# Optimization experiments

Hardware: AMD Instinct MI355X
Metric: run time of the kernel (lower is better)

## Reference

```python
import jax, jax.numpy as jnp
import numpy as np

N = 100000          # nodes
E = 1600000         # edges
F = 128             # raw node features
D = 16              # embedding_dim (per-head out channels)
H = 8               # heads
NEG_SLOPE = 0.2     # GATConv leaky_relu slope
EPS = 1e-16         # PyG softmax denominator eps


def _glorot(key, shape):
    fan_in, fan_out = shape[0], shape[-1]
    lim = np.sqrt(6.0 / (fan_in + fan_out))
    return jax.random.uniform(key, shape, jnp.float32, -lim, lim)


def setup_inputs() -> dict:
    key = jax.random.key(0)
    ks = jax.random.split(key, 24)
    x = jax.random.normal(ks[0], (N, F), jnp.float32)
    edge_index = jax.random.randint(ks[1], (2, E), 0, N, jnp.int64)
    HD = H * D
    return {
        "x": x,
        "edge_index": edge_index,
        # attribute embedding Linear(F, D)
        "W_emb": _glorot(ks[2], (F, D)), "b_emb": jnp.zeros((D,), jnp.float32),
        # GAT layer 0: in=D, out=D per head
        "W0": _glorot(ks[3], (D, HD)),
        "as0": _glorot(ks[4], (H, D)), "ad0": _glorot(ks[5], (H, D)),
        "b0": jnp.zeros((HD,), jnp.float32),
        # GAT layer 1: in=H*D, out=D per head
        "W1": _glorot(ks[6], (HD, HD)),
        "as1": _glorot(ks[7], (H, D)), "ad1": _glorot(ks[8], (H, D)),
        "b1": jnp.zeros((HD,), jnp.float32),
        "Wy1": _glorot(ks[9], (HD, 1)), "by1": jnp.zeros((1,), jnp.float32),
        "Wy0": _glorot(ks[10], (HD, 1)), "by0": jnp.zeros((1,), jnp.float32),
        # classifier Linear(HD, D) -> ReLU -> Linear(D, 1) -> Sigmoid
        "Wc1": _glorot(ks[11], (HD, D)), "bc1": jnp.zeros((D,), jnp.float32),
        "Wc2": _glorot(ks[12], (D, 1)), "bc2": jnp.zeros((1,), jnp.float32),
    }


def _gat_conv(h, src, dst, W, att_src, att_dst, bias):
    # h: [N, in] -> out: [N, H*D]; src/dst already include self-loops
    g = (h @ W).reshape(N, H, D)                                   # [N,H,D]
    a_src = jnp.einsum('nhd,hd->nh', g, att_src)                   # [N,H]
    a_dst = jnp.einsum('nhd,hd->nh', g, att_dst)                   # [N,H]
    logits = jax.nn.leaky_relu(a_src[src] + a_dst[dst], NEG_SLOPE) # [Et,H]
    m = jax.ops.segment_max(logits, dst, num_segments=N)           # [N,H]
    ex = jnp.exp(logits - m[dst])
    denom = jax.ops.segment_sum(ex, dst, num_segments=N)           # [N,H]
    alpha = ex / (denom[dst] + EPS)                                # [Et,H]
    msg = g[src] * alpha[..., None]                                # [Et,H,D]
    out = jax.ops.segment_sum(msg, dst, num_segments=N)            # [N,H,D]
    return out.reshape(N, H * D) + bias


def reference(x, edge_index, W_emb, b_emb, W0, as0, ad0, b0,
              W1, as1, ad1, b1, Wy1, by1, Wy0, by0, Wc1, bc1, Wc2, bc2):
    # add self loops (PyG GATConv default)
    loop = jnp.arange(N, dtype=edge_index.dtype)
    src = jnp.concatenate([edge_index[0], loop])
    dst = jnp.concatenate([edge_index[1], loop])

    h = x @ W_emb + b_emb                        # [N,D]
    h = _gat_conv(h, src, dst, W0, as0, ad0, b0) # [N,H*D]
    h = _gat_conv(h, src, dst, W1, as1, ad1, b1) # [N,H*D]

    y1 = h @ Wy1 + by1
    y0 = h @ Wy0 + by0
    causal_effect = y1 - y0                      # [N,1]
    propensity = jax.nn.sigmoid(jax.nn.relu(h @ Wc1 + bc1) @ Wc2 + bc2)  # [N,1]
    return causal_effect, propensity
```

## Files before the change

kernel.cpp:

```cpp
#include <hip/hip_runtime.h>
#include <hip/hip_fp16.h>
#include <math.h>

#define N_NODES 100000
#define E_EDGES 1600000
#define F_IN 128
#define D_DIM 16
#define H_HEADS 8
#define HD 128
#define NEG_SLOPE 0.2f

#define SCAN_BLOCKS 256
#define SCAN_T 256
#define SCAN_CH ((N_NODES + SCAN_BLOCKS - 1) / SCAN_BLOCKS)

#define NTILES ((N_NODES + 63) / 64)

#define NB_E 196
#define EB 128
#define CH_E ((E_EDGES + EB - 1) / EB)

__global__ __launch_bounds__(256) void embed_kernel(
        const float* __restrict__ x, const float* __restrict__ W,
        const float* __restrict__ b, __half* __restrict__ h0) {
    __shared__ float Ws[F_IN * D_DIM];
    __shared__ float bs[D_DIM];
    __shared__ float xs[16][F_IN + 1];
    int t = threadIdx.x;
    for (int i = t; i < F_IN * D_DIM; i += 256) Ws[i] = W[i];
    if (t < D_DIM) bs[t] = b[t];
    __syncthreads();
    for (int base = blockIdx.x * 16; base < N_NODES; base += gridDim.x * 16) {
        int cnt = min(16, N_NODES - base);
        __syncthreads();
        for (int i = t; i < cnt * F_IN; i += 256) {
            int nn = i >> 7, k = i & 127;
            xs[nn][k] = x[(size_t)(base + nn) * F_IN + k];
        }
        __syncthreads();
        int nn = t >> 4, c = t & 15;
        if (nn < cnt) {
            float a0 = 0.f, a1 = 0.f, a2 = 0.f, a3 = 0.f;
            #pragma unroll
            for (int k = 0; k < F_IN; k += 4) {
                a0 += xs[nn][k + 0] * Ws[(k + 0) * D_DIM + c];
                a1 += xs[nn][k + 1] * Ws[(k + 1) * D_DIM + c];
                a2 += xs[nn][k + 2] * Ws[(k + 2) * D_DIM + c];
                a3 += xs[nn][k + 3] * Ws[(k + 3) * D_DIM + c];
            }
            h0[(size_t)(base + nn) * D_DIM + c] =
                __float2half((a0 + a1) + (a2 + a3) + bs[c]);
        }
    }
}

__global__ __launch_bounds__(256) void precompute_kernel(
        const float* __restrict__ W0, const float* __restrict__ W1,
        const float* __restrict__ as0, const float* __restrict__ ad0,
        const float* __restrict__ b0,
        float* __restrict__ W_fused, float* __restrict__ u_s,
        float* __restrict__ u_d, float* __restrict__ bvec) {
    int t = threadIdx.x;
    if (t < 128) {
        int h = t >> 4, c = t & 15;
        float ss = 0.f, sd = 0.f;
        for (int dp = 0; dp < 16; ++dp) {
            float w = W0[c * HD + h * 16 + dp];
            ss += w * as0[h * 16 + dp];
            sd += w * ad0[h * 16 + dp];
        }
        u_s[t] = ss; u_d[t] = sd;
        float bb = 0.f;
        for (int k = 0; k < HD; ++k) bb += b0[k] * W1[k * HD + t];
        bvec[t] = bb;
    }
    for (int idx = t; idx < HD * HD; idx += 256) {
        int i = idx >> 7, j = idx & 127;
        int h = i >> 4, c = i & 15;
        float s = 0.f;
        for (int dp = 0; dp < 16; ++dp)
            s += W0[c * HD + h * 16 + dp] * W1[(h * 16 + dp) * HD + j];
        W_fused[idx] = s;
    }
}

__global__ __launch_bounds__(256) void attdot0_kernel(
        const __half* __restrict__ h0, const float* __restrict__ u_s,
        const float* __restrict__ u_d,
        float* __restrict__ a_s, float* __restrict__ a_d) {
    __shared__ float us[128], ud[128];
    int t = threadIdx.x;
    if (t < 128) { us[t] = u_s[t]; ud[t] = u_d[t]; }
    __syncthreads();
    int gidx = blockIdx.x * 256 + t;
    int n = gidx >> 3, h = gidx & 7;
    if (n >= N_NODES) return;
    const __half2* hp = (const __half2*)(h0 + (size_t)n * D_DIM);
    float ss = 0.f, sd = 0.f;
    #pragma unroll
    for (int c2 = 0; c2 < 8; ++c2) {
        float2 f = __half22float2(hp[c2]);
        ss += f.x * us[h * 16 + 2 * c2] + f.y * us[h * 16 + 2 * c2 + 1];
        sd += f.x * ud[h * 16 + 2 * c2] + f.y * ud[h * 16 + 2 * c2 + 1];
    }
    a_s[n * 8 + h] = ss;
    a_d[n * 8 + h] = sd;
}

__global__ __launch_bounds__(256) void transform_fused_kernel(
        const __half* __restrict__ m, const float* __restrict__ W,
        const float* __restrict__ bvec,
        const float* __restrict__ att_s, const float* __restrict__ att_d,
        __half* __restrict__ g, float* __restrict__ a_src, float* __restrict__ a_dst) {
    __shared__ float Ws[128][64];
    __shared__ float hs[64][128 + 4];
    int t = threadIdx.x;
    int cq = t & 15;
    int nq = t >> 4;

    for (int item = blockIdx.x; item < NTILES * 2; item += gridDim.x) {
        int tile = item >> 1;
        int coff = (item & 1) << 6;
        int nbase = tile << 6;
        __syncthreads();
        for (int i = t; i < 128 * 64; i += 256)
            Ws[i >> 6][i & 63] = W[(size_t)(i >> 6) * HD + coff + (i & 63)];
        for (int i = t; i < (128 << 6); i += 256) {
            int r = i >> 7, k = i & 127;
            int n = nbase + r; if (n >= N_NODES) n = N_NODES - 1;
            hs[r][k] = __half2float(m[(size_t)n * HD + k]);
        }
        __syncthreads();

        float acc[4][4] = {{0.f}};
        #pragma unroll 2
        for (int k = 0; k < 128; k += 4) {
            float4 w0 = *(const float4*)&Ws[k + 0][cq << 2];
            float4 w1 = *(const float4*)&Ws[k + 1][cq << 2];
            float4 w2 = *(const float4*)&Ws[k + 2][cq << 2];
            float4 w3 = *(const float4*)&Ws[k + 3][cq << 2];
            #pragma unroll
            for (int j = 0; j < 4; ++j) {
                float4 hv = *(const float4*)&hs[(nq << 2) + j][k];
                acc[j][0] += hv.x * w0.x + hv.y * w1.x + hv.z * w2.x + hv.w * w3.x;
                acc[j][1] += hv.x * w0.y + hv.y * w1.y + hv.z * w2.y + hv.w * w3.y;
                acc[j][2] += hv.x * w0.z + hv.y * w1.z + hv.z * w2.z + hv.w * w3.z;
                acc[j][3] += hv.x * w0.w + hv.y * w1.w + hv.z * w2.w + hv.w * w3.w;
            }
        }

        int c0 = coff + (cq << 2);
        float bq0 = bvec[c0], bq1 = bvec[c0 + 1], bq2 = bvec[c0 + 2], bq3 = bvec[c0 + 3];
        float as0 = att_s[c0], as1 = att_s[c0 + 1], as2 = att_s[c0 + 2], as3 = att_s[c0 + 3];
        float ad0 = att_d[c0], ad1 = att_d[c0 + 1], ad2 = att_d[c0 + 2], ad3 = att_d[c0 + 3];
        int head = c0 >> 4;
        #pragma unroll
        for (int j = 0; j < 4; ++j) {
            int n = nbase + (nq << 2) + j;
            float g0 = acc[j][0] + bq0, g1v = acc[j][1] + bq1;
            float g2 = acc[j][2] + bq2, g3v = acc[j][3] + bq3;
            float ps = g0 * as0 + g1v * as1 + g2 * as2 + g3v * as3;
            float pd = g0 * ad0 + g1v * ad1 + g2 * ad2 + g3v * ad3;
            ps += __shfl_xor(ps, 1); ps += __shfl_xor(ps, 2);
            pd += __shfl_xor(pd, 1); pd += __shfl_xor(pd, 2);
            if (n < N_NODES) {
                union { __half2 h2[2]; uint2 u; } pk;
                pk.h2[0] = __floats2half2_rn(g0, g1v);
                pk.h2[1] = __floats2half2_rn(g2, g3v);
                *(uint2*)&g[(size_t)n * HD + c0] = pk.u;
                if ((cq & 3) == 0) {
                    a_src[(size_t)n * H_HEADS + head] = ps;
                    a_dst[(size_t)n * H_HEADS + head] = pd;
                }
            }
        }
    }
}

__global__ __launch_bounds__(256) void hist_kernel(
        const int* __restrict__ ei, int* __restrict__ deg) {
    int e = blockIdx.x * 256 + threadIdx.x;
    if (e < E_EDGES) atomicAdd(&deg[ei[E_EDGES + e]], 1);
}

__global__ __launch_bounds__(SCAN_T) void block_sum_kernel(
        const int* __restrict__ deg, int* __restrict__ bsum) {
    int b = blockIdx.x, t = threadIdx.x;
    int lo = b * SCAN_CH, hi = min(lo + SCAN_CH, N_NODES);
    int s = 0;
    for (int i = lo + t; i < hi; i += SCAN_T) s += deg[i];
    #pragma unroll
    for (int m = 1; m < 64; m <<= 1) s += __shfl_xor(s, m);
    __shared__ int ws[SCAN_T / 64];
    if ((t & 63) == 0) ws[t >> 6] = s;
    __syncthreads();
    if (t == 0) {
        int tot = 0;
        #pragma unroll
        for (int w = 0; w < SCAN_T / 64; ++w) tot += ws[w];
        bsum[b] = tot;
    }
}

__global__ __launch_bounds__(SCAN_BLOCKS) void offset_scan_kernel(
        const int* __restrict__ bsum, int* __restrict__ boff) {
    __shared__ int tmp[SCAN_BLOCKS];
    int t = threadIdx.x;
    int v = bsum[t];
    tmp[t] = v;
    __syncthreads();
    int val = v;
    for (int off = 1; off < SCAN_BLOCKS; off <<= 1) {
        int o = (t >= off) ? tmp[t - off] : 0;
        __syncthreads();
        val += o;
        tmp[t] = val;
        __syncthreads();
    }
    boff[t] = val - v;
}

__global__ __launch_bounds__(SCAN_T) void row_ptr_kernel(
        const int* __restrict__ deg, const int* __restrict__ boff,
        int* __restrict__ row_ptr) {
    int b = blockIdx.x, t = threadIdx.x;
    int lo = b * SCAN_CH, hi = min(lo + SCAN_CH, N_NODES);
    __shared__ int tmp[SCAN_T];
    __shared__ int carry;
    if (t == 0) carry = boff[b];
    __syncthreads();
    for (int base = lo; base < hi; base += SCAN_T) {
        int i = base + t;
        int v = (i < hi) ? deg[i] : 0;
        tmp[t] = v;
        __syncthreads();
        int val = v;
        for (int off = 1; off < SCAN_T; off <<= 1) {
            int o = (t >= off) ? tmp[t - off] : 0;
            __syncthreads();
            val += o;
            tmp[t] = val;
            __syncthreads();
        }
        int excl = val - v + carry;
        if (i < hi) row_ptr[i] = excl;
        __syncthreads();
        if (t == SCAN_T - 1) carry = carry + val;
        __syncthreads();
    }
    if (b == SCAN_BLOCKS - 1 && t == 0) row_ptr[N_NODES] = carry;
}

__global__ __launch_bounds__(256) void ebfill_init_kernel(
        const int* __restrict__ row_ptr, int* __restrict__ ebfill) {
    int t = threadIdx.x;
    if (t < NB_E) ebfill[t] = row_ptr[t * 512];
}

__global__ __launch_bounds__(256) void edge_partition_kernel(
        const int* __restrict__ ei, int* __restrict__ ebfill,
        int* __restrict__ epack) {
    __shared__ int lh[NB_E];
    __shared__ int lbase[NB_E];
    int b = blockIdx.x, t = threadIdx.x;
    int lo = b * CH_E, hi = min(lo + CH_E, E_EDGES);
    for (int i = t; i < NB_E; i += 256) lh[i] = 0;
    __syncthreads();
    for (int e = lo + t; e < hi; e += 256)
        atomicAdd(&lh[ei[E_EDGES + e] >> 9], 1);
    __syncthreads();
    if (t < NB_E) lbase[t] = atomicAdd(&ebfill[t], lh[t]);
    __syncthreads();
    for (int e = lo + t; e < hi; e += 256) {
        int s = ei[e], d = ei[E_EDGES + e];
        int p = atomicAdd(&lbase[d >> 9], 1);
        epack[p] = (s << 9) | (d & 511);
    }
}

__global__ __launch_bounds__(256) void bucket_col_kernel(
        const int* __restrict__ row_ptr, const int* __restrict__ epack,
        int* __restrict__ col) {
    __shared__ int lfill[512];
    int b = blockIdx.x, t = threadIdx.x;
    int nb0 = b * 512;
    for (int k = t; k < 512; k += 256)
        lfill[k] = row_ptr[min(nb0 + k, N_NODES)];
    __syncthreads();
    int lo = row_ptr[nb0];
    int hi = row_ptr[min(nb0 + 512, N_NODES)];
    for (int i = lo + t; i < hi; i += 256) {
        int v = epack[i];
        int p = atomicAdd(&lfill[v & 511], 1);
        col[p] = ((unsigned)v) >> 9;
    }
}

__global__ __launch_bounds__(256) void bucket_hist_kernel(
        const int* __restrict__ deg, int* __restrict__ bcount) {
    __shared__ int lh[64];
    int b = blockIdx.x, t = threadIdx.x;
    if (t < 64) lh[t] = 0;
    __syncthreads();
    int lo = b * SCAN_CH, hi = min(lo + SCAN_CH, N_NODES);
    for (int i = lo + t; i < hi; i += 256)
        atomicAdd(&lh[min(deg[i], 63)], 1);
    __syncthreads();
    if (t < 64) bcount[t * SCAN_BLOCKS + b] = lh[t];
}

__global__ __launch_bounds__(1024) void bucket_scan_kernel(
        const int* __restrict__ bcount, int* __restrict__ boffs) {
    __shared__ int part[1024];
    int t = threadIdx.x;
    int base = t * 16;
    int v[16]; int s = 0;
    #pragma unroll
    for (int k = 0; k < 16; ++k) { v[k] = bcount[base + k]; s += v[k]; }
    part[t] = s;
    __syncthreads();
    int val = s;
    for (int off = 1; off < 1024; off <<= 1) {
        int o = (t >= off) ? part[t - off] : 0;
        __syncthreads();
        val += o;
        part[t] = val;
        __syncthreads();
    }
    int run = val - s;
    #pragma unroll
    for (int k = 0; k < 16; ++k) { boffs[base + k] = run; run += v[k]; }
}

__global__ __launch_bounds__(256) void bucket_scatter_kernel(
        const int* __restrict__ deg, const int* __restrict__ boffs,
        int* __restrict__ perm) {
    __shared__ int lbase[64];
    int b = blockIdx.x, t = threadIdx.x;
    if (t < 64) lbase[t] = boffs[t * SCAN_BLOCKS + b];
    __syncthreads();
    int lo = b * SCAN_CH, hi = min(lo + SCAN_CH, N_NODES);
    for (int i = lo + t; i < hi; i += 256) {
        int p = atomicAdd(&lbase[min(deg[i], 63)], 1);
        perm[p] = i;
    }
}

__global__ __launch_bounds__(256) void gat_aggr0_kernel(
        const int* __restrict__ perm,
        const int* __restrict__ row_ptr, const int* __restrict__ col,
        const float* __restrict__ a_src, const float* __restrict__ a_dst,
        const __half* __restrict__ h0, __half* __restrict__ m) {
    int wv = threadIdx.x >> 6, lane = threadIdx.x & 63;
    int grp = lane >> 4;
    int sub = lane & 15;
    int cq = sub & 3;
    int hp = sub >> 2;
    int slot = blockIdx.x * 16 + wv * 4 + grp;
    bool dvalid = slot < N_NODES;
    int d = perm[dvalid ? slot : N_NODES - 1];

    int i0 = row_ptr[d], end = row_ptr[d + 1];
    int deg = dvalid ? (end - i0) : 0;
    float2 ad = *(const float2*)(a_dst + (size_t)d * 8 + 2 * hp);

    float acc0[4], acc1[4];
    float den0, den1;
    {
        float2 as = *(const float2*)(a_src + (size_t)d * 8 + 2 * hp);
        float l0 = as.x + ad.x; l0 = fmaxf(l0, NEG_SLOPE * l0);
        float l1 = as.y + ad.y; l1 = fmaxf(l1, NEG_SLOPE * l1);
        float w0 = __expf(l0), w1 = __expf(l1);
        uint2 hv = *(const uint2*)(h0 + (size_t)d * D_DIM + 4 * cq);
        float2 fa = __half22float2(*(__half2*)&hv.x);
        float2 fb = __half22float2(*(__half2*)&hv.y);
        acc0[0] = w0 * fa.x; acc0[1] = w0 * fa.y;
        acc0[2] = w0 * fb.x; acc0[3] = w0 * fb.y;
        acc1[0] = w1 * fa.x; acc1[1] = w1 * fa.y;
        acc1[2] = w1 * fb.x; acc1[3] = w1 * fb.y;
        den0 = w0; den1 = w1;
    }

    int md = deg;
    md = max(md, __shfl_xor(md, 16));
    md = max(md, __shfl_xor(md, 32));

    int colv = 0;
    #define EDGE_K(EL)                                                       \
    {                                                                        \
        int el_ = (EL);                                                      \
        int s = __shfl(colv, (grp << 4) | (el_ & 15));                       \
        float2 as = *(const float2*)(a_src + (size_t)s * 8 + 2 * hp);        \
        float l0 = as.x + ad.x; l0 = fmaxf(l0, NEG_SLOPE * l0);              \
        float l1 = as.y + ad.y; l1 = fmaxf(l1, NEG_SLOPE * l1);              \
        float w0 = (el_ < deg) ? __expf(l0) : 0.f;                           \
        float w1 = (el_ < deg) ? __expf(l1) : 0.f;                           \
        uint2 hv = *(const uint2*)(h0 + (size_t)s * D_DIM + 4 * cq);         \
        float2 fa = __half22float2(*(__half2*)&hv.x);                        \
        float2 fb = __half22float2(*(__half2*)&hv.y);                        \
        acc0[0] += w0 * fa.x; acc0[1] += w0 * fa.y;                          \
        acc0[2] += w0 * fb.x; acc0[3] += w0 * fb.y;                          \
        acc1[0] += w1 * fa.x; acc1[1] += w1 * fa.y;                          \
        acc1[2] += w1 * fb.x; acc1[3] += w1 * fb.y;                          \
        den0 += w0; den1 += w1;                                              \
    }

    for (int el = 0; el < md; el += 4) {
        if ((el & 15) == 0) {
            int ci = i0 + el + sub;
            ci = min(ci, end - 1);
            ci = max(ci, 0);
            colv = col[ci];
        }
        EDGE_K(el);
        EDGE_K(el + 1);
        EDGE_K(el + 2);
        EDGE_K(el + 3);
    }
    #undef EDGE_K

    float inv0 = 1.f / (den0 + 1e-16f);
    float inv1 = 1.f / (den1 + 1e-16f);
    if (dvalid) {
        union { __half2 h2[2]; uint2 u; } p0, p1;
        p0.h2[0] = __floats2half2_rn(acc0[0] * inv0, acc0[1] * inv0);
        p0.h2[1] = __floats2half2_rn(acc0[2] * inv0, acc0[3] * inv0);
        p1.h2[0] = __floats2half2_rn(acc1[0] * inv1, acc1[1] * inv1);
        p1.h2[1] = __floats2half2_rn(acc1[2] * inv1, acc1[3] * inv1);
        *(uint2*)(m + (size_t)d * HD + (2 * hp) * 16 + 4 * cq)       = p0.u;
        *(uint2*)(m + (size_t)d * HD + (2 * hp + 1) * 16 + 4 * cq)   = p1.u;
    }
}

__global__ __launch_bounds__(256) void gat_aggr1_kernel(
        const int* __restrict__ perm,
        const int* __restrict__ row_ptr, const int* __restrict__ col,
        const float* __restrict__ a_src, const float* __restrict__ a_dst,
        const __half* __restrict__ g, const float* __restrict__ bias,
        float* __restrict__ out,
        const float* __restrict__ Wy1, const float* __restrict__ by1,
        const float* __restrict__ Wy0, const float* __restrict__ by0,
        const float* __restrict__ Wc1, const float* __restrict__ bc1,
        const float* __restrict__ Wc2, const float* __restrict__ bc2) {
    int wv = threadIdx.x >> 6, lane = threadIdx.x & 63;
    int grp = lane >> 4;
    int sub = lane & 15;
    int hh  = sub >> 1;
    int slot = blockIdx.x * 16 + wv * 4 + grp;
    bool dvalid = slot < N_NODES;
    int d = perm[dvalid ? slot : N_NODES - 1];

    int i0 = row_ptr[d], end = row_ptr[d + 1];
    int deg = dvalid ? (end - i0) : 0;
    float ad = a_dst[d * 8 + hh];

    float acc[8];
    float den;
    {
        float a = a_src[d * 8 + hh] + ad;
        a = fmaxf(a, NEG_SLOPE * a);
        float w = __expf(a);
        uint4 rv = *(const uint4*)(g + (size_t)d * HD + (sub << 3));
        float2 f0 = __half22float2(*(__half2*)&rv.x);
        float2 f1 = __half22float2(*(__half2*)&rv.y);
        float2 f2 = __half22float2(*(__half2*)&rv.z);
        float2 f3 = __half22float2(*(__half2*)&rv.w);
        acc[0] = w * f0.x; acc[1] = w * f0.y;
        acc[2] = w * f1.x; acc[3] = w * f1.y;
        acc[4] = w * f2.x; acc[5] = w * f2.y;
        acc[6] = w * f3.x; acc[7] = w * f3.y;
        den = w;
    }

    int md = deg;
    md = max(md, __shfl_xor(md, 16));
    md = max(md, __shfl_xor(md, 32));

    int colv = 0;
    #define EDGE_K(EL)                                                       \
    {                                                                        \
        int el_ = (EL);                                                      \
        int s = __shfl(colv, (grp << 4) | (el_ & 15));                       \
        float a = a_src[s * 8 + hh] + ad;                                    \
        a = fmaxf(a, NEG_SLOPE * a);                                         \
        float w = (el_ < deg) ? __expf(a) : 0.f;                             \
        uint4 rv = *(const uint4*)(g + (size_t)s * HD + (sub << 3));         \
        float2 f0 = __half22float2(*(__half2*)&rv.x);                        \
        float2 f1 = __half22float2(*(__half2*)&rv.y);                        \
        float2 f2 = __half22float2(*(__half2*)&rv.z);                        \
        float2 f3 = __half22float2(*(__half2*)&rv.w);                        \
        acc[0] += w * f0.x; acc[1] += w * f0.y;                              \
        acc[2] += w * f1.x; acc[3] += w * f1.y;                              \
        acc[4] += w * f2.x; acc[5] += w * f2.y;                              \
        acc[6] += w * f3.x; acc[7] += w * f3.y;                              \
        den += w;                                                            \
    }

    for (int el = 0; el < md; el += 4) {
        if ((el & 15) == 0) {
            int ci = i0 + el + sub;
            ci = min(ci, end - 1);
            ci = max(ci, 0);
            colv = col[ci];
        }
        EDGE_K(el);
        EDGE_K(el + 1);
        EDGE_K(el + 2);
        EDGE_K(el + 3);
    }
    #undef EDGE_K

    float inv = 1.f / (den + 1e-16f);
    int c0 = sub << 3;
    float h[8];
    #pragma unroll
    for (int k = 0; k < 8; ++k) h[k] = acc[k] * inv + bias[c0 + k];

    float p = 0.f;
    #pragma unroll
    for (int k = 0; k < 8; ++k)
        p += h[k] * (Wy1[c0 + k] - Wy0[c0 + k]);
    p += __shfl_xor(p, 1); p += __shfl_xor(p, 2);
    p += __shfl_xor(p, 4); p += __shfl_xor(p, 8);
    float acc2 = 0.f;
    #pragma unroll
    for (int j = 0; j < D_DIM; ++j) {
        float q = 0.f;
        #pragma unroll
        for (int k = 0; k < 8; ++k)
            q += h[k] * Wc1[(c0 + k) * D_DIM + j];
        q += __shfl_xor(q, 1); q += __shfl_xor(q, 2);
        q += __shfl_xor(q, 4); q += __shfl_xor(q, 8);
        float z = q + bc1[j];
        z = (z > 0.f) ? z : 0.f;
        acc2 += z * Wc2[j];
    }
    if (sub == 0 && dvalid) {
        out[d] = p + by1[0] - by0[0];
        out[N_NODES + d] = 1.f / (1.f + __expf(-(acc2 + bc2[0])));
    }
}

extern "C" void kernel_launch(void* const* d_in, const int* in_sizes, int n_in,
                              void* d_out, int out_size, void* d_ws, size_t ws_size,
                              hipStream_t stream) {
    const float* x     = (const float*)d_in[0];
    const int*   ei    = (const int*)  d_in[1];
    const float* W_emb = (const float*)d_in[2];
    const float* b_emb = (const float*)d_in[3];
    const float* W0    = (const float*)d_in[4];
    const float* as0   = (const float*)d_in[5];
    const float* ad0   = (const float*)d_in[6];
    const float* b0    = (const float*)d_in[7];
    const float* W1    = (const float*)d_in[8];
    const float* as1   = (const float*)d_in[9];
    const float* ad1   = (const float*)d_in[10];
    const float* b1    = (const float*)d_in[11];
    const float* Wy1   = (const float*)d_in[12];
    const float* by1   = (const float*)d_in[13];
    const float* Wy0   = (const float*)d_in[14];
    const float* by0   = (const float*)d_in[15];
    const float* Wc1   = (const float*)d_in[16];
    const float* bc1   = (const float*)d_in[17];
    const float* Wc2   = (const float*)d_in[18];
    const float* bc2   = (const float*)d_in[19];
    float* out = (float*)d_out;

    float* ws    = (float*)d_ws;
    __half* mH   = (__half*)ws;
    __half* gH   = (__half*)(ws + (size_t)N_NODES * 64);
    __half* h0h  = (__half*)(ws + (size_t)N_NODES * 128);
    float* a_s   = ws + (size_t)N_NODES * 136;
    float* a_d   = a_s + (size_t)N_NODES * 8;
    float* Wf    = a_d + (size_t)N_NODES * 8;
    float* u_s   = Wf + 16384;
    float* u_d   = u_s + 128;
    float* bvec  = u_d + 128;
    int*   deg     = (int*)(bvec + 128);
    int*   row_ptr = deg + N_NODES;
    int*   bsum    = row_ptr + (N_NODES + 1);
    int*   boff    = bsum + SCAN_BLOCKS;
    int*   bcount  = boff + SCAN_BLOCKS;
    int*   boffs   = bcount + 64 * SCAN_BLOCKS;
    int*   perm    = boffs + 64 * SCAN_BLOCKS;
    int*   col     = perm + N_NODES;
    int*   epack   = col + E_EDGES;
    int*   ebfill  = epack + E_EDGES;

    int edgeBlocks = (E_EDGES + 255) / 256;
    int aggrBlocks = (N_NODES + 15) / 16;

    hipMemsetAsync(deg, 0, (size_t)N_NODES * sizeof(int), stream);
    hipLaunchKernelGGL(hist_kernel, dim3(edgeBlocks), dim3(256), 0, stream, ei, deg);
    hipLaunchKernelGGL(block_sum_kernel, dim3(SCAN_BLOCKS), dim3(SCAN_T), 0, stream,
                       deg, bsum);
    hipLaunchKernelGGL(offset_scan_kernel, dim3(1), dim3(SCAN_BLOCKS), 0, stream,
                       bsum, boff);
    hipLaunchKernelGGL(row_ptr_kernel, dim3(SCAN_BLOCKS), dim3(SCAN_T), 0, stream,
                       deg, boff, row_ptr);

    hipLaunchKernelGGL(ebfill_init_kernel, dim3(1), dim3(256), 0, stream,
                       row_ptr, ebfill);
    hipLaunchKernelGGL(edge_partition_kernel, dim3(EB), dim3(256), 0, stream,
                       ei, ebfill, epack);
    hipLaunchKernelGGL(bucket_col_kernel, dim3(NB_E), dim3(256), 0, stream,
                       row_ptr, epack, col);

    hipLaunchKernelGGL(bucket_hist_kernel, dim3(SCAN_BLOCKS), dim3(256), 0, stream,
                       deg, bcount);
    hipLaunchKernelGGL(bucket_scan_kernel, dim3(1), dim3(1024), 0, stream,
                       bcount, boffs);
    hipLaunchKernelGGL(bucket_scatter_kernel, dim3(SCAN_BLOCKS), dim3(256), 0, stream,
                       deg, boffs, perm);

    hipLaunchKernelGGL(embed_kernel, dim3(512), dim3(256), 0, stream,
                       x, W_emb, b_emb, h0h);
    hipLaunchKernelGGL(precompute_kernel, dim3(1), dim3(256), 0, stream,
                       W0, W1, as0, ad0, b0, Wf, u_s, u_d, bvec);

    hipLaunchKernelGGL(attdot0_kernel, dim3((N_NODES * 8 + 255) / 256), dim3(256),
                       0, stream, h0h, u_s, u_d, a_s, a_d);
    hipLaunchKernelGGL(gat_aggr0_kernel, dim3(aggrBlocks), dim3(256), 0, stream,
                       perm, row_ptr, col, a_s, a_d, h0h, mH);

    hipLaunchKernelGGL(transform_fused_kernel, dim3(1024), dim3(256), 0, stream,
                       mH, Wf, bvec, as1, ad1, gH, a_s, a_d);
    hipLaunchKernelGGL(gat_aggr1_kernel, dim3(aggrBlocks), dim3(256), 0, stream,
                       perm, row_ptr, col, a_s, a_d, gH, b1, out,
                       Wy1, by1, Wy0, by0, Wc1, bc1, Wc2, bc2);
}
```

Measured before the change: 456.9 us.

## Build CSR via two-pass bucket partition, dropping global degree histogram and scans

Result: faster. 415.9 us (-9.0%).

```diff
diff --git a/kernel.cpp b/kernel.cpp
--- a/kernel.cpp
+++ b/kernel.cpp
@@ -11,7 +11,6 @@
 #define NEG_SLOPE 0.2f
 
 #define SCAN_BLOCKS 256
-#define SCAN_T 256
 #define SCAN_CH ((N_NODES + SCAN_BLOCKS - 1) / SCAN_BLOCKS)
 
 #define NTILES ((N_NODES + 63) / 64)
@@ -19,6 +18,7 @@
 #define NB_E 196
 #define EB 128
 #define CH_E ((E_EDGES + EB - 1) / EB)
+#define NBB (NB_E * EB)
 
 __global__ __launch_bounds__(256) void embed_kernel(
         const float* __restrict__ x, const float* __restrict__ W,
@@ -177,99 +177,47 @@
     }
 }
 
-__global__ __launch_bounds__(256) void hist_kernel(
-        const int* __restrict__ ei, int* __restrict__ deg) {
-    int e = blockIdx.x * 256 + threadIdx.x;
-    if (e < E_EDGES) atomicAdd(&deg[ei[E_EDGES + e]], 1);
-}
-
-__global__ __launch_bounds__(SCAN_T) void block_sum_kernel(
-        const int* __restrict__ deg, int* __restrict__ bsum) {
+__global__ __launch_bounds__(256) void epart_count_kernel(
+        const int* __restrict__ ei, int* __restrict__ bcountE) {
+    __shared__ int lh[NB_E];
     int b = blockIdx.x, t = threadIdx.x;
-    int lo = b * SCAN_CH, hi = min(lo + SCAN_CH, N_NODES);
+    int lo = b * CH_E, hi = min(lo + CH_E, E_EDGES);
+    for (int i = t; i < NB_E; i += 256) lh[i] = 0;
+    __syncthreads();
+    for (int e = lo + t; e < hi; e += 256)
+        atomicAdd(&lh[ei[E_EDGES + e] >> 9], 1);
+    __syncthreads();
+    for (int i = t; i < NB_E; i += 256) bcountE[i * EB + b] = lh[i];
+}
+
+__global__ __launch_bounds__(1024) void escan_kernel(
+        const int* __restrict__ bcountE, int* __restrict__ ebaseBB) {
+    __shared__ int part[1024];
+    int t = threadIdx.x;
+    int lo = t * 25, hi = min(lo + 25, NBB);
     int s = 0;
-    for (int i = lo + t; i < hi; i += SCAN_T) s += deg[i];
-    #pragma unroll
-    for (int m = 1; m < 64; m <<= 1) s += __shfl_xor(s, m);
-    __shared__ int ws[SCAN_T / 64];
-    if ((t & 63) == 0) ws[t >> 6] = s;
-    __syncthreads();
-    if (t == 0) {
-        int tot = 0;
-        #pragma unroll
-        for (int w = 0; w < SCAN_T / 64; ++w) tot += ws[w];
-        bsum[b] = tot;
-    }
-}
-
-__global__ __launch_bounds__(SCAN_BLOCKS) void offset_scan_kernel(
-        const int* __restrict__ bsum, int* __restrict__ boff) {
-    __shared__ int tmp[SCAN_BLOCKS];
-    int t = threadIdx.x;
-    int v = bsum[t];
-    tmp[t] = v;
-    __syncthreads();
-    int val = v;
-    for (int off = 1; off < SCAN_BLOCKS; off <<= 1) {
-        int o = (t >= off) ? tmp[t - off] : 0;
+    for (int i = lo; i < hi; ++i) s += bcountE[i];
+    part[t] = s;
+    __syncthreads();
+    int val = s;
+    for (int off = 1; off < 1024; off <<= 1) {
+        int o = (t >= off) ? part[t - off] : 0;
         __syncthreads();
         val += o;
-        tmp[t] = val;
-        __syncthreads();
-    }
-    boff[t] = val - v;
-}
-
-__global__ __launch_bounds__(SCAN_T) void row_ptr_kernel(
-        const int* __restrict__ deg, const int* __restrict__ boff,
-        int* __restrict__ row_ptr) {
-    int b = blockIdx.x, t = threadIdx.x;
-    int lo = b * SCAN_CH, hi = min(lo + SCAN_CH, N_NODES);
-    __shared__ int tmp[SCAN_T];
-    __shared__ int carry;
-    if (t == 0) carry = boff[b];
-    __syncthreads();
-    for (int base = lo; base < hi; base += SCAN_T) {
-        int i = base + t;
-        int v = (i < hi) ? deg[i] : 0;
-        tmp[t] = v;
-        __syncthreads();
-        int val = v;
-        for (int off = 1; off < SCAN_T; off <<= 1) {
-            int o = (t >= off) ? tmp[t - off] : 0;
-            __syncthreads();
-            val += o;
-            tmp[t] = val;
-            __syncthreads();
-        }
-        int excl = val - v + carry;
-        if (i < hi) row_ptr[i] = excl;
-        __syncthreads();
-        if (t == SCAN_T - 1) carry = carry + val;
-        __syncthreads();
-    }
-    if (b == SCAN_BLOCKS - 1 && t == 0) row_ptr[N_NODES] = carry;
-}
-
-__global__ __launch_bounds__(256) void ebfill_init_kernel(
-        const int* __restrict__ row_ptr, int* __restrict__ ebfill) {
-    int t = threadIdx.x;
-    if (t < NB_E) ebfill[t] = row_ptr[t * 512];
-}
-
-__global__ __launch_bounds__(256) void edge_partition_kernel(
-        const int* __restrict__ ei, int* __restrict__ ebfill,
+        part[t] = val;
+        __syncthreads();
+    }
+    int run = val - s;
+    for (int i = lo; i < hi; ++i) { ebaseBB[i] = run; run += bcountE[i]; }
+}
+
+__global__ __launch_bounds__(256) void epart_write_kernel(
+        const int* __restrict__ ei, const int* __restrict__ ebaseBB,
         int* __restrict__ epack) {
-    __shared__ int lh[NB_E];
     __shared__ int lbase[NB_E];
     int b = blockIdx.x, t = threadIdx.x;
     int lo = b * CH_E, hi = min(lo + CH_E, E_EDGES);
-    for (int i = t; i < NB_E; i += 256) lh[i] = 0;
-    __syncthreads();
-    for (int e = lo + t; e < hi; e += 256)
-        atomicAdd(&lh[ei[E_EDGES + e] >> 9], 1);
-    __syncthreads();
-    if (t < NB_E) lbase[t] = atomicAdd(&ebfill[t], lh[t]);
+    for (int i = t; i < NB_E; i += 256) lbase[i] = ebaseBB[i * EB + b];
     __syncthreads();
     for (int e = lo + t; e < hi; e += 256) {
         int s = ei[e], d = ei[E_EDGES + e];
@@ -278,17 +226,40 @@
     }
 }
 
-__global__ __launch_bounds__(256) void bucket_col_kernel(
-        const int* __restrict__ row_ptr, const int* __restrict__ epack,
-        int* __restrict__ col) {
+__global__ __launch_bounds__(256) void bucket_build_kernel(
+        const int* __restrict__ ebaseBB, const int* __restrict__ epack,
+        int* __restrict__ row_ptr, int* __restrict__ col) {
+    __shared__ int lh[512];
+    __shared__ int sc[256];
     __shared__ int lfill[512];
     int b = blockIdx.x, t = threadIdx.x;
+    int lo = ebaseBB[b * EB];
+    int hi = (b == NB_E - 1) ? E_EDGES : ebaseBB[(b + 1) * EB];
+    lh[t] = 0; lh[t + 256] = 0;
+    __syncthreads();
+    for (int i = lo + t; i < hi; i += 256)
+        atomicAdd(&lh[epack[i] & 511], 1);
+    __syncthreads();
+    int c0 = lh[2 * t], c1 = lh[2 * t + 1];
+    int pairSum = c0 + c1;
+    sc[t] = pairSum;
+    __syncthreads();
+    int val = pairSum;
+    for (int off = 1; off < 256; off <<= 1) {
+        int o = (t >= off) ? sc[t - off] : 0;
+        __syncthreads();
+        val += o;
+        sc[t] = val;
+        __syncthreads();
+    }
+    int excl2 = val - pairSum;
+    int p0 = lo + excl2, p1 = lo + excl2 + c0;
+    lfill[2 * t] = p0;
+    lfill[2 * t + 1] = p1;
     int nb0 = b * 512;
-    for (int k = t; k < 512; k += 256)
-        lfill[k] = row_ptr[min(nb0 + k, N_NODES)];
-    __syncthreads();
-    int lo = row_ptr[nb0];
-    int hi = row_ptr[min(nb0 + 512, N_NODES)];
+    if (nb0 + 2 * t     <= N_NODES) row_ptr[nb0 + 2 * t]     = p0;
+    if (nb0 + 2 * t + 1 <= N_NODES) row_ptr[nb0 + 2 * t + 1] = p1;
+    __syncthreads();
     for (int i = lo + t; i < hi; i += 256) {
         int v = epack[i];
         int p = atomicAdd(&lfill[v & 511], 1);
@@ -297,14 +268,16 @@
 }
 
 __global__ __launch_bounds__(256) void bucket_hist_kernel(
-        const int* __restrict__ deg, int* __restrict__ bcount) {
+        const int* __restrict__ row_ptr, int* __restrict__ bcount) {
     __shared__ int lh[64];
     int b = blockIdx.x, t = threadIdx.x;
     if (t < 64) lh[t] = 0;
     __syncthreads();
     int lo = b * SCAN_CH, hi = min(lo + SCAN_CH, N_NODES);
-    for (int i = lo + t; i < hi; i += 256)
-        atomicAdd(&lh[min(deg[i], 63)], 1);
+    for (int i = lo + t; i < hi; i += 256) {
+        int dg = row_ptr[i + 1] - row_ptr[i];
+        atomicAdd(&lh[min(dg, 63)], 1);
+    }
     __syncthreads();
     if (t < 64) bcount[t * SCAN_BLOCKS + b] = lh[t];
 }
@@ -333,7 +306,7 @@
 }
 
 __global__ __launch_bounds__(256) void bucket_scatter_kernel(
-        const int* __restrict__ deg, const int* __restrict__ boffs,
+        const int* __restrict__ row_ptr, const int* __restrict__ boffs,
         int* __restrict__ perm) {
     __shared__ int lbase[64];
     int b = blockIdx.x, t = threadIdx.x;
@@ -341,7 +314,8 @@
     __syncthreads();
     int lo = b * SCAN_CH, hi = min(lo + SCAN_CH, N_NODES);
     for (int i = lo + t; i < hi; i += 256) {
-        int p = atomicAdd(&lbase[min(deg[i], 63)], 1);
+        int dg = row_ptr[i + 1] - row_ptr[i];
+        int p = atomicAdd(&lbase[min(dg, 63)], 1);
         perm[p] = i;
     }
 }
@@ -576,42 +550,32 @@
     float* u_s   = Wf + 16384;
     float* u_d   = u_s + 128;
     float* bvec  = u_d + 128;
-    int*   deg     = (int*)(bvec + 128);
-    int*   row_ptr = deg + N_NODES;
-    int*   bsum    = row_ptr + (N_NODES + 1);
-    int*   boff    = bsum + SCAN_BLOCKS;
-    int*   bcount  = boff + SCAN_BLOCKS;
+    int*   row_ptr = (int*)(bvec + 128);
+    int*   bcountE = row_ptr + (N_NODES + 1);
+    int*   ebaseBB = bcountE + NBB;
+    int*   bcount  = ebaseBB + NBB;
     int*   boffs   = bcount + 64 * SCAN_BLOCKS;
     int*   perm    = boffs + 64 * SCAN_BLOCKS;
     int*   col     = perm + N_NODES;
     int*   epack   = col + E_EDGES;
-    int*   ebfill  = epack + E_EDGES;
-
-    int edgeBlocks = (E_EDGES + 255) / 256;
+
     int aggrBlocks = (N_NODES + 15) / 16;
 
-    hipMemsetAsync(deg, 0, (size_t)N_NODES * sizeof(int), stream);
-    hipLaunchKernelGGL(hist_kernel, dim3(edgeBlocks), dim3(256), 0, stream, ei, deg);
-    hipLaunchKernelGGL(block_sum_kernel, dim3(SCAN_BLOCKS), dim3(SCAN_T), 0, stream,
-                       deg, bsum);
-    hipLaunchKernelGGL(offset_scan_kernel, dim3(1), dim3(SCAN_BLOCKS), 0, stream,
-                       bsum, boff);
-    hipLaunchKernelGGL(row_ptr_kernel, dim3(SCAN_BLOCKS), dim3(SCAN_T), 0, stream,
-                       deg, boff, row_ptr);
-
-    hipLaunchKernelGGL(ebfill_init_kernel, dim3(1), dim3(256), 0, stream,
-                       row_ptr, ebfill);
-    hipLaunchKernelGGL(edge_partition_kernel, dim3(EB), dim3(256), 0, stream,
-                       ei, ebfill, epack);
-    hipLaunchKernelGGL(bucket_col_kernel, dim3(NB_E), dim3(256), 0, stream,
-                       row_ptr, epack, col);
+    hipLaunchKernelGGL(epart_count_kernel, dim3(EB), dim3(256), 0, stream,
+                       ei, bcountE);
+    hipLaunchKernelGGL(escan_kernel, dim3(1), dim3(1024), 0, stream,
+                       bcountE, ebaseBB);
+    hipLaunchKernelGGL(epart_write_kernel, dim3(EB), dim3(256), 0, stream,
+                       ei, ebaseBB, epack);
+    hipLaunchKernelGGL(bucket_build_kernel, dim3(NB_E), dim3(256), 0, stream,
+                       ebaseBB, epack, row_ptr, col);
 
     hipLaunchKernelGGL(bucket_hist_kernel, dim3(SCAN_BLOCKS), dim3(256), 0, stream,
-                       deg, bcount);
+                       row_ptr, bcount);
     hipLaunchKernelGGL(bucket_scan_kernel, dim3(1), dim3(1024), 0, stream,
                        bcount, boffs);
     hipLaunchKernelGGL(bucket_scatter_kernel, dim3(SCAN_BLOCKS), dim3(256), 0, stream,
-                       deg, boffs, perm);
+                       row_ptr, boffs, perm);
 
     hipLaunchKernelGGL(embed_kernel, dim3(512), dim3(256), 0, stream,
                        x, W_emb, b_emb, h0h);
```
